# Kernel optimization log

Hardware: AMD Instinct MI355X
Metric: run time of the kernel (lower is better)

The kernel has to match this reference:

```python
import jax, jax.numpy as jnp
import numpy as np

D_LOB = 128
D_HAWKES = 32
N_HEADS = 4
HEAD_DIM = D_LOB // N_HEADS
LN_EPS = 1e-5


def setup_inputs() -> dict:
    key = jax.random.key(0)
    ks = jax.random.split(key, 10)
    B, T = 8, 2048
    s = lambda fan_in: 1.0 / np.sqrt(fan_in)
    return {
        "lob": jax.random.normal(ks[0], (B, T, D_LOB), dtype=jnp.float32),
        "hawkes": jax.random.normal(ks[1], (B, T, D_HAWKES), dtype=jnp.float32),
        # hawkes_proj: Linear(d_hawkes, d_lob)
        "Wp": jax.random.uniform(ks[2], (D_LOB, D_HAWKES), jnp.float32, -s(D_HAWKES), s(D_HAWKES)),
        "bp": jnp.zeros((D_LOB,), jnp.float32),
        # MultiheadAttention packed in-projection (3*d_lob, d_lob) and out-projection
        "Win": jax.random.uniform(ks[3], (3 * D_LOB, D_LOB), jnp.float32, -s(D_LOB), s(D_LOB)),
        "bin_": jnp.zeros((3 * D_LOB,), jnp.float32),
        "Wo": jax.random.uniform(ks[4], (D_LOB, D_LOB), jnp.float32, -s(D_LOB), s(D_LOB)),
        "bo": jnp.zeros((D_LOB,), jnp.float32),
        # LayerNorm affine params
        "gamma": jnp.ones((D_LOB,), jnp.float32),
        "beta": jnp.zeros((D_LOB,), jnp.float32),
    }


def reference(lob, hawkes, Wp, bp, Win, bin_, Wo, bo, gamma, beta):
    B, T, _ = lob.shape
    # hawkes_proj
    h = hawkes @ Wp.T + bp  # (B, T, d_lob)
    # packed QKV projection (query=lob, key=value=h)
    q = lob @ Win[:D_LOB].T + bin_[:D_LOB]
    k = h @ Win[D_LOB:2 * D_LOB].T + bin_[D_LOB:2 * D_LOB]
    v = h @ Win[2 * D_LOB:].T + bin_[2 * D_LOB:]
    # split heads -> (B, H, T, hd)
    split = lambda x: x.reshape(B, T, N_HEADS, HEAD_DIM).transpose(0, 2, 1, 3)
    q, k, v = split(q), split(k), split(v)
    scale = 1.0 / np.sqrt(HEAD_DIM).astype(np.float32)
    scores = jnp.einsum("bhqd,bhkd->bhqk", q * scale, k)  # (B, H, T, T)
    attn = jax.nn.softmax(scores, axis=-1)
    # dropout(p=0.1) omitted: reference is eval/inference mode
    ctx = jnp.einsum("bhqk,bhkd->bhqd", attn, v)  # (B, H, T, hd)
    ctx = ctx.transpose(0, 2, 1, 3).reshape(B, T, D_LOB)
    fused = ctx @ Wo.T + bo
    # residual + LayerNorm
    x = lob + fused
    mu = jnp.mean(x, axis=-1, keepdims=True)
    var = jnp.mean(jnp.square(x - mu), axis=-1, keepdims=True)
    out = (x - mu) * jax.lax.rsqrt(var + LN_EPS) * gamma + beta
    attn_w = jnp.mean(attn, axis=1)  # average over heads (B, T, T)
    return out, attn_w
```

## Files before the change

kernel.cpp:

```cpp
#include <hip/hip_runtime.h>
#include <hip/hip_bf16.h>
#include <math.h>

#define TT 2048
#define BB 8
#define DD 128
#define HH 4
#define BT (BB*TT)
#define BH (BB*HH)
#define SCALE 0.1767766952966369f
#define S2LOG (SCALE * 1.4426950408889634f)

typedef __attribute__((ext_vector_type(8))) short short8;
typedef __attribute__((ext_vector_type(4))) short short4v;
typedef __attribute__((ext_vector_type(4))) float f32x4;
typedef __attribute__((ext_vector_type(4))) unsigned u32x4;
typedef __hip_bfloat16 bf16;

#define MFMA16(a,b,c) __builtin_amdgcn_mfma_f32_16x16x32_bf16(a,b,c,0,0,0)

static __device__ inline short8 ldg8(const bf16* p) {
  return *reinterpret_cast<const short8*>(p);
}
static __device__ inline short4v ldg4(const bf16* p) {
  return *reinterpret_cast<const short4v*>(p);
}
static __device__ inline short f2bs(float x) {
  bf16 h = __float2bfloat16(x);
  return *reinterpret_cast<short*>(&h);
}
static __device__ inline unsigned cvtpk(float lo, float hi) {
  unsigned r;
  asm("v_cvt_pk_bf16_f32 %0, %1, %2" : "=v"(r) : "v"(lo), "v"(hi));
  return r;
}
static __device__ inline short8 ldcvt8(const float* p) {
  f32x4 f0 = *reinterpret_cast<const f32x4*>(p);
  f32x4 f1 = *reinterpret_cast<const f32x4*>(p + 4);
  short8 r;
  #pragma unroll
  for (int i = 0; i < 4; ++i) { r[i] = f2bs(f0[i]); r[4+i] = f2bs(f1[i]); }
  return r;
}

__global__ __launch_bounds__(256) void proj_kernel(
    const float* __restrict__ lob, const float* __restrict__ hawkes,
    const float* __restrict__ Wp, const float* __restrict__ bp,
    const float* __restrict__ Win, const float* __restrict__ binp,
    bf16* __restrict__ qg, bf16* __restrict__ kg, bf16* __restrict__ vtg) {
  __shared__ bf16 hT[32*136];
  __shared__ bf16 sK[32*136];
  __shared__ bf16 vT[128*40];
  int tid = threadIdx.x;
  int wave = tid >> 6, lane = tid & 63;
  int lr = lane & 15, lq = lane >> 4;
  int r0 = blockIdx.x * 32;
  int b  = r0 >> 11, t0 = r0 & 2047;
  f32x4 z = {0.f,0.f,0.f,0.f};

  short8 alob[2][4], ahk[2];
  #pragma unroll
  for (int mt = 0; mt < 2; ++mt) {
    const float* lp = lob + (size_t)(r0 + mt*16 + lr)*128;
    #pragma unroll
    for (int kt = 0; kt < 4; ++kt) alob[mt][kt] = ldcvt8(lp + kt*32 + lq*8);
    ahk[mt] = ldcvt8(hawkes + (size_t)(r0 + mt*16 + lr)*32 + lq*8);
  }

  for (int nt = wave; nt < 8; nt += 4) {
    int cn = nt*16;
    short8 bfrag = ldcvt8(Wp + (size_t)(cn + lr)*32 + lq*8);
    float bias = bp[cn + lr];
    #pragma unroll
    for (int mt = 0; mt < 2; ++mt) {
      f32x4 c = MFMA16(ahk[mt], bfrag, z);
      #pragma unroll
      for (int r = 0; r < 4; ++r)
        hT[(mt*16 + lq*4 + r)*136 + cn + lr] = __float2bfloat16(c[r] + bias);
    }
  }
  __syncthreads();

  short8 ah[2][4];
  #pragma unroll
  for (int mt = 0; mt < 2; ++mt)
    #pragma unroll
    for (int kt = 0; kt < 4; ++kt)
      ah[mt][kt] = *reinterpret_cast<const short8*>(&hT[(mt*16 + lr)*136 + kt*32 + lq*8]);
  __syncthreads();

  for (int nt = wave; nt < 24; nt += 4) {
    int which = nt >> 3;
    int c = (nt & 7)*16 + lr;
    const float* wrow = Win + (size_t)(which*128 + c)*128;
    float bias = binp[which*128 + c];
    f32x4 acc0 = z, acc1 = z;
    #pragma unroll
    for (int kt = 0; kt < 4; ++kt) {
      short8 bfrag = ldcvt8(wrow + kt*32 + lq*8);
      if (which == 0) {
        acc0 = MFMA16(alob[0][kt], bfrag, acc0);
        acc1 = MFMA16(alob[1][kt], bfrag, acc1);
      } else {
        acc0 = MFMA16(ah[0][kt], bfrag, acc0);
        acc1 = MFMA16(ah[1][kt], bfrag, acc1);
      }
    }
    #pragma unroll
    for (int mt = 0; mt < 2; ++mt) {
      f32x4 acc = mt ? acc1 : acc0;
      #pragma unroll
      for (int r = 0; r < 4; ++r) {
        int row = mt*16 + lq*4 + r;
        float val = acc[r] + bias;
        if (which == 0)      hT[row*136 + c] = __float2bfloat16(val);
        else if (which == 1) sK[row*136 + c] = __float2bfloat16(val);
        else                 vT[c*40 + row]  = __float2bfloat16(val);
      }
    }
  }
  __syncthreads();

  {
    int head = tid >> 6, tt = (tid >> 1) & 31, half = tid & 1;
    const bf16* sq = &hT[tt*136 + head*32 + half*16];
    const bf16* sk = &sK[tt*136 + head*32 + half*16];
    bf16* qdst = qg + ((size_t)(b*HH + head)*TT + t0 + tt)*32 + half*16;
    bf16* kdst = kg + ((size_t)(b*HH + head)*TT + t0 + tt)*32 + half*16;
    *reinterpret_cast<short8*>(qdst)     = *reinterpret_cast<const short8*>(sq);
    *reinterpret_cast<short8*>(qdst + 8) = *reinterpret_cast<const short8*>(sq + 8);
    *reinterpret_cast<short8*>(kdst)     = *reinterpret_cast<const short8*>(sk);
    *reinterpret_cast<short8*>(kdst + 8) = *reinterpret_cast<const short8*>(sk + 8);
  }
  {
    int dd = tid >> 1, half = tid & 1;
    int bh = b*HH + (dd >> 5);
    short8 s0 = *reinterpret_cast<const short8*>(&vT[dd*40 + half*16]);
    short8 s1 = *reinterpret_cast<const short8*>(&vT[dd*40 + half*16 + 8]);
    bf16* dst = vtg + ((size_t)bh*32 + (dd & 31))*TT + t0 + half*16;
    *reinterpret_cast<short8*>(dst) = s0;
    *reinterpret_cast<short8*>(dst + 8) = s1;
  }
}

__global__ __launch_bounds__(512) void attn_kernel(const bf16* __restrict__ qg,
    const bf16* __restrict__ kg, const bf16* __restrict__ vtg,
    float* __restrict__ attn_out, const float* __restrict__ lobf,
    const float* __restrict__ Wo, const float* __restrict__ bo,
    const float* __restrict__ gamma, const float* __restrict__ beta,
    float* __restrict__ outg) {
  int wgid = (blockIdx.x & 7)*64 + (blockIdx.x >> 3);
  int b = wgid >> 6, qt = wgid & 63;
  int tid = threadIdx.x;
  int wave = tid >> 6, lane = tid & 63;
  int head = wave & 3, half = wave >> 2;
  int lr = lane & 15, lq = lane >> 4;
  int bh = b*HH + head;
  __shared__ float plds[2][4][32*36];
  const bf16* qp = qg + ((size_t)bh*TT + (size_t)qt*32)*32;
  const bf16* kb = kg + (size_t)bh*TT*32;
  const bf16* vb = vtg + (size_t)bh*32*TT;
  f32x4 z = {0.f,0.f,0.f,0.f};

  short8 aq0 = ldg8(qp + lr*32 + lq*8);
  short8 aq1 = ldg8(qp + (16+lr)*32 + lq*8);

  float rs0 = 0.f, rs1 = 0.f;
  {
    short8 kA0 = ldg8(kb + (size_t)(half*32 + lr)*32 + lq*8);
    short8 kA1 = ldg8(kb + (size_t)(half*32 + 16 + lr)*32 + lq*8);
    short8 kB0, kB1;
#define P1STEP(KC0, KC1, KN0, KN1, NCC) { \
    int nc_ = (NCC); \
    KN0 = ldg8(kb + (size_t)(nc_*32 + lr)*32 + lq*8); \
    KN1 = ldg8(kb + (size_t)(nc_*32 + 16 + lr)*32 + lq*8); \
    f32x4 sa0 = MFMA16(KC0, aq0, z), sb0 = MFMA16(KC1, aq0, z); \
    f32x4 sa1 = MFMA16(KC0, aq1, z), sb1 = MFMA16(KC1, aq1, z); \
    _Pragma("unroll") for (int r = 0; r < 4; ++r) { \
      rs0 += exp2f(sa0[r]*S2LOG) + exp2f(sb0[r]*S2LOG); \
      rs1 += exp2f(sa1[r]*S2LOG) + exp2f(sb1[r]*S2LOG); } }
    #pragma unroll 1
    for (int i = 0; i < 32; i += 2) {
      P1STEP(kA0, kA1, kB0, kB1, 2*(i+1) + half);
      P1STEP(kB0, kB1, kA0, kA1, (i+2 < 32) ? 2*(i+2) + half : half);
    }
#undef P1STEP
  }
  rs0 += __shfl_xor(rs0, 16, 64); rs0 += __shfl_xor(rs0, 32, 64);
  rs1 += __shfl_xor(rs1, 16, 64); rs1 += __shfl_xor(rs1, 32, 64);
  float* sdl = &plds[0][0][0];
  if (lq == 0) { sdl[wave*32 + lr] = rs0; sdl[wave*32 + 16 + lr] = rs1; }
  __syncthreads();
  float lb0 = -log2f(sdl[head*32 + lr]      + sdl[(4+head)*32 + lr]);
  float lb1 = -log2f(sdl[head*32 + 16 + lr] + sdl[(4+head)*32 + 16 + lr]);
  __syncthreads();

  f32x4 acc00 = z, acc01 = z, acc10 = z, acc11 = z;
  float* awr = attn_out + (size_t)(b*TT + qt*32)*TT;
  int mloc = tid & 255;
  int mq = mloc >> 3, mk = (mloc & 7)*4;

  short8 kA0 = ldg8(kb + (size_t)(half*32 + lr)*32 + lq*8);
  short8 kA1 = ldg8(kb + (size_t)(half*32 + 16 + lr)*32 + lq*8);
  short4v vA00 = ldg4(vb + (size_t)lr*TT + half*32 + lq*4);
  short4v vA01 = ldg4(vb + (size_t)lr*TT + half*32 + 16 + lq*4);
  short4v vA10 = ldg4(vb + (size_t)(16+lr)*TT + half*32 + lq*4);
  short4v vA11 = ldg4(vb + (size_t)(16+lr)*TT + half*32 + 16 + lq*4);
  short8 kB0, kB1; short4v vB00, vB01, vB10, vB11;

#define P2STEP(KC, KC0, KC1, VC00, VC01, VC10, VC11, KN0, KN1, VN00, VN01, VN10, VN11, NCC) { \
    int kc_ = (KC); int nc_ = (NCC); \
    KN0 = ldg8(kb + (size_t)(nc_*32 + lr)*32 + lq*8); \
    KN1 = ldg8(kb + (size_t)(nc_*32 + 16 + lr)*32 + lq*8); \
    VN00 = ldg4(vb + (size_t)lr*TT + nc_*32 + lq*4); \
    VN01 = ldg4(vb + (size_t)lr*TT + nc_*32 + 16 + lq*4); \
    VN10 = ldg4(vb + (size_t)(16+lr)*TT + nc_*32 + lq*4); \
    VN11 = ldg4(vb + (size_t)(16+lr)*TT + nc_*32 + 16 + lq*4); \
    f32x4 s00 = MFMA16(KC0, aq0, z), s10 = MFMA16(KC1, aq0, z); \
    f32x4 s01 = MFMA16(KC0, aq1, z), s11 = MFMA16(KC1, aq1, z); \
    f32x4 p00, p10, p01, p11; \
    _Pragma("unroll") for (int r = 0; r < 4; ++r) { \
      p00[r] = exp2f(fmaf(s00[r], S2LOG, lb0)); \
      p10[r] = exp2f(fmaf(s10[r], S2LOG, lb0)); \
      p01[r] = exp2f(fmaf(s01[r], S2LOG, lb1)); \
      p11[r] = exp2f(fmaf(s11[r], S2LOG, lb1)); } \
    { float* pw = &plds[half][head][0]; \
      *reinterpret_cast<f32x4*>(pw + lr*36 + lq*4)           = p00; \
      *reinterpret_cast<f32x4*>(pw + lr*36 + 16 + lq*4)      = p10; \
      *reinterpret_cast<f32x4*>(pw + (16+lr)*36 + lq*4)      = p01; \
      *reinterpret_cast<f32x4*>(pw + (16+lr)*36 + 16 + lq*4) = p11; } \
    u32x4 ua_, ub_; \
    ua_[0] = cvtpk(p00[0], p00[1]); ua_[1] = cvtpk(p00[2], p00[3]); \
    ua_[2] = cvtpk(p10[0], p10[1]); ua_[3] = cvtpk(p10[2], p10[3]); \
    ub_[0] = cvtpk(p01[0], p01[1]); ub_[1] = cvtpk(p01[2], p01[3]); \
    ub_[2] = cvtpk(p11[0], p11[1]); ub_[3] = cvtpk(p11[2], p11[3]); \
    short8 ap0 = *reinterpret_cast<short8*>(&ua_); \
    short8 ap1 = *reinterpret_cast<short8*>(&ub_); \
    __syncthreads(); \
    { const float* pr = &plds[half][0][0]; \
      f32x4 mv = *reinterpret_cast<const f32x4*>(pr + mq*36 + mk); \
      mv = mv + *reinterpret_cast<const f32x4*>(pr + 1152 + mq*36 + mk); \
      mv = mv + *reinterpret_cast<const f32x4*>(pr + 2304 + mq*36 + mk); \
      mv = mv + *reinterpret_cast<const f32x4*>(pr + 3456 + mq*36 + mk); \
      *reinterpret_cast<f32x4*>(awr + (size_t)mq*TT + kc_*32 + mk) = mv * 0.25f; } \
    short8 vf0, vf1; \
    _Pragma("unroll") for (int j = 0; j < 4; ++j) { \
      vf0[j] = VC00[j]; vf0[4+j] = VC01[j]; \
      vf1[j] = VC10[j]; vf1[4+j] = VC11[j]; } \
    acc00 = MFMA16(ap0, vf0, acc00); acc01 = MFMA16(ap0, vf1, acc01); \
    acc10 = MFMA16(ap1, vf0, acc10); acc11 = MFMA16(ap1, vf1, acc11); \
    __syncthreads(); }

  #pragma unroll 1
  for (int i = 0; i < 32; i += 2) {
    P2STEP(2*i + half, kA0, kA1, vA00, vA01, vA10, vA11,
           kB0, kB1, vB00, vB01, vB10, vB11, 2*(i+1) + half);
    P2STEP(2*(i+1) + half, kB0, kB1, vB00, vB01, vB10, vB11,
           kA0, kA1, vA00, vA01, vA10, vA11, (i+2 < 32) ? 2*(i+2) + half : half);
  }
#undef P2STEP

  size_t rowbase = (size_t)(b*TT) + (size_t)qt*32;
  float* sRed = &plds[0][0][0];
  {
    float* myR = sRed + half*4224;
    #pragma unroll
    for (int m = 0; m < 2; ++m) {
      f32x4 a0 = m ? acc10 : acc00;
      f32x4 a1 = m ? acc11 : acc01;
      #pragma unroll
      for (int r = 0; r < 4; ++r) {
        int row = m*16 + lq*4 + r;
        myR[row*132 + head*32 + lr]      = a0[r];
        myR[row*132 + head*32 + 16 + lr] = a1[r];
      }
    }
  }
  __syncthreads();
  for (int idx = tid; idx < 4096; idx += 512) {
    int row = idx >> 7, d = idx & 127;
    sRed[row*132 + d] += sRed[4224 + row*132 + d];
  }
  __syncthreads();
  float* sX  = sRed;
  float* sX2 = sRed + 4224;
  short8 actx[2][4];
  #pragma unroll
  for (int mt = 0; mt < 2; ++mt)
    #pragma unroll
    for (int kt = 0; kt < 4; ++kt) {
      const float* cp = &sX[(mt*16 + lr)*132 + kt*32 + lq*8];
      f32x4 c0 = *reinterpret_cast<const f32x4*>(cp);
      f32x4 c1 = *reinterpret_cast<const f32x4*>(cp + 4);
      u32x4 u;
      u[0] = cvtpk(c0[0], c0[1]); u[1] = cvtpk(c0[2], c0[3]);
      u[2] = cvtpk(c1[0], c1[1]); u[3] = cvtpk(c1[2], c1[3]);
      actx[mt][kt] = *reinterpret_cast<short8*>(&u);
    }
  {
    int nt = wave;
    f32x4 acc0 = z, acc1 = z;
    #pragma unroll
    for (int kt = 0; kt < 4; ++kt) {
      short8 bfrag = ldcvt8(Wo + (size_t)(nt*16 + lr)*128 + kt*32 + lq*8);
      acc0 = MFMA16(actx[0][kt], bfrag, acc0);
      acc1 = MFMA16(actx[1][kt], bfrag, acc1);
    }
    int d = nt*16 + lr;
    float bias = bo[d];
    #pragma unroll
    for (int mt = 0; mt < 2; ++mt) {
      f32x4 acc = mt ? acc1 : acc0;
      #pragma unroll
      for (int r = 0; r < 4; ++r) {
        int row = mt*16 + lq*4 + r;
        sX2[row*132 + d] = acc[r] + bias + lobf[(rowbase + row)*128 + d];
      }
    }
  }
  __syncthreads();
  {
    int row = tid >> 4, j = tid & 15;
    const float* xp = &sX2[row*132 + j*8];
    f32x4 x0 = *reinterpret_cast<const f32x4*>(xp);
    f32x4 x1 = *reinterpret_cast<const f32x4*>(xp + 4);
    float sum = 0.f, sq = 0.f;
    #pragma unroll
    for (int e = 0; e < 4; ++e) {
      sum += x0[e] + x1[e];
      sq  += x0[e]*x0[e] + x1[e]*x1[e];
    }
    #pragma unroll
    for (int mdx = 1; mdx < 16; mdx <<= 1) {
      sum += __shfl_xor(sum, mdx, 64);
      sq  += __shfl_xor(sq,  mdx, 64);
    }
    float mu = sum * (1.0f/128.0f);
    float rstd = rsqrtf(sq*(1.0f/128.0f) - mu*mu + 1e-5f);
    float* op = outg + (rowbase + row)*128 + j*8;
    f32x4 o0, o1;
    #pragma unroll
    for (int e = 0; e < 4; ++e) {
      int d = j*8 + e;
      o0[e] = (x0[e] - mu)*rstd*gamma[d]   + beta[d];
      o1[e] = (x1[e] - mu)*rstd*gamma[d+4] + beta[d+4];
    }
    *reinterpret_cast<f32x4*>(op)     = o0;
    *reinterpret_cast<f32x4*>(op + 4) = o1;
  }
}

extern "C" void kernel_launch(void* const* d_in, const int* in_sizes, int n_in,
                              void* d_out, int out_size, void* d_ws, size_t ws_size,
                              hipStream_t stream) {
  const float* lob    = (const float*)d_in[0];
  const float* hawkes = (const float*)d_in[1];
  const float* Wp     = (const float*)d_in[2];
  const float* bp     = (const float*)d_in[3];
  const float* Win    = (const float*)d_in[4];
  const float* binp   = (const float*)d_in[5];
  const float* Wo     = (const float*)d_in[6];
  const float* bo     = (const float*)d_in[7];
  const float* gamma  = (const float*)d_in[8];
  const float* beta   = (const float*)d_in[9];
  float* outg = (float*)d_out;
  float* attn_out = outg + (size_t)BT*128;

  char* ws = (char*)d_ws;
  bf16*  qg   = (bf16*)(ws);
  bf16*  kg   = (bf16*)(ws + (size_t)4*1024*1024);
  bf16*  vtg  = (bf16*)(ws + (size_t)8*1024*1024);

  proj_kernel<<<BT/32, 256, 0, stream>>>(lob, hawkes, Wp, bp, Win, binp, qg, kg, vtg);
  attn_kernel<<<BB*(TT/32), 512, 0, stream>>>(qg, kg, vtg, attn_out,
                                              lob, Wo, bo, gamma, beta, outg);
}
```

Before: 275.6 us.

## Halve query tile to 16 rows, double-buffer bf16 probabilities in LDS, drop one barrier

Each attention workgroup now handles 16 query rows instead of 32, so the grid doubles to 1024 blocks. Per-head probabilities are stored to LDS as packed bf16 instead of fp32, and a ping-pong buffer lets each step use one barrier instead of two. The head-averaged attention weights are rebuilt from the bf16 values. This aims to improve occupancy and cut LDS traffic and sync stalls, at the cost of re-reading K and V twice as often and slightly lower precision in attn_w.

```diff
diff --git a/kernel.cpp b/kernel.cpp
--- a/kernel.cpp
+++ b/kernel.cpp
@@ -14,7 +14,9 @@
 typedef __attribute__((ext_vector_type(8))) short short8;
 typedef __attribute__((ext_vector_type(4))) short short4v;
 typedef __attribute__((ext_vector_type(4))) float f32x4;
+typedef __attribute__((ext_vector_type(2))) float f32x2;
 typedef __attribute__((ext_vector_type(4))) unsigned u32x4;
+typedef __attribute__((ext_vector_type(2))) unsigned u32x2;
 typedef __hip_bfloat16 bf16;
 
 #define MFMA16(a,b,c) __builtin_amdgcn_mfma_f32_16x16x32_bf16(a,b,c,0,0,0)
@@ -149,23 +151,22 @@
     const float* __restrict__ Wo, const float* __restrict__ bo,
     const float* __restrict__ gamma, const float* __restrict__ beta,
     float* __restrict__ outg) {
-  int wgid = (blockIdx.x & 7)*64 + (blockIdx.x >> 3);
-  int b = wgid >> 6, qt = wgid & 63;
+  int wgid = (blockIdx.x & 7)*128 + (blockIdx.x >> 3);
+  int b = wgid >> 7, qt = wgid & 127;
   int tid = threadIdx.x;
   int wave = tid >> 6, lane = tid & 63;
   int head = wave & 3, half = wave >> 2;
   int lr = lane & 15, lq = lane >> 4;
   int bh = b*HH + head;
-  __shared__ float plds[2][4][32*36];
-  const bf16* qp = qg + ((size_t)bh*TT + (size_t)qt*32)*32;
+  __shared__ unsigned plds[4608];
+  const bf16* qp = qg + ((size_t)bh*TT + (size_t)qt*16)*32;
   const bf16* kb = kg + (size_t)bh*TT*32;
   const bf16* vb = vtg + (size_t)bh*32*TT;
   f32x4 z = {0.f,0.f,0.f,0.f};
 
-  short8 aq0 = ldg8(qp + lr*32 + lq*8);
-  short8 aq1 = ldg8(qp + (16+lr)*32 + lq*8);
-
-  float rs0 = 0.f, rs1 = 0.f;
+  short8 aq = ldg8(qp + lr*32 + lq*8);
+
+  float rs = 0.f;
   {
     short8 kA0 = ldg8(kb + (size_t)(half*32 + lr)*32 + lq*8);
     short8 kA1 = ldg8(kb + (size_t)(half*32 + 16 + lr)*32 + lq*8);
@@ -174,31 +175,30 @@
     int nc_ = (NCC); \
     KN0 = ldg8(kb + (size_t)(nc_*32 + lr)*32 + lq*8); \
     KN1 = ldg8(kb + (size_t)(nc_*32 + 16 + lr)*32 + lq*8); \
-    f32x4 sa0 = MFMA16(KC0, aq0, z), sb0 = MFMA16(KC1, aq0, z); \
-    f32x4 sa1 = MFMA16(KC0, aq1, z), sb1 = MFMA16(KC1, aq1, z); \
-    _Pragma("unroll") for (int r = 0; r < 4; ++r) { \
-      rs0 += exp2f(sa0[r]*S2LOG) + exp2f(sb0[r]*S2LOG); \
-      rs1 += exp2f(sa1[r]*S2LOG) + exp2f(sb1[r]*S2LOG); } }
+    f32x4 sa = MFMA16(KC0, aq, z), sb = MFMA16(KC1, aq, z); \
+    _Pragma("unroll") for (int r = 0; r < 4; ++r) \
+      rs += exp2f(sa[r]*S2LOG) + exp2f(sb[r]*S2LOG); }
     #pragma unroll 1
-    for (int i = 0; i < 32; i += 2) {
-      P1STEP(kA0, kA1, kB0, kB1, 2*(i+1) + half);
-      P1STEP(kB0, kB1, kA0, kA1, (i+2 < 32) ? 2*(i+2) + half : half);
+    for (int s = 0; s < 32; s += 2) {
+      P1STEP(kA0, kA1, kB0, kB1, 2*(s+1) + half);
+      P1STEP(kB0, kB1, kA0, kA1, (s+2 < 32) ? 2*(s+2) + half : half);
     }
 #undef P1STEP
   }
-  rs0 += __shfl_xor(rs0, 16, 64); rs0 += __shfl_xor(rs0, 32, 64);
-  rs1 += __shfl_xor(rs1, 16, 64); rs1 += __shfl_xor(rs1, 32, 64);
-  float* sdl = &plds[0][0][0];
-  if (lq == 0) { sdl[wave*32 + lr] = rs0; sdl[wave*32 + 16 + lr] = rs1; }
-  __syncthreads();
-  float lb0 = -log2f(sdl[head*32 + lr]      + sdl[(4+head)*32 + lr]);
-  float lb1 = -log2f(sdl[head*32 + 16 + lr] + sdl[(4+head)*32 + 16 + lr]);
-  __syncthreads();
-
-  f32x4 acc00 = z, acc01 = z, acc10 = z, acc11 = z;
-  float* awr = attn_out + (size_t)(b*TT + qt*32)*TT;
-  int mloc = tid & 255;
-  int mq = mloc >> 3, mk = (mloc & 7)*4;
+  rs += __shfl_xor(rs, 16, 64);
+  rs += __shfl_xor(rs, 32, 64);
+  float* sdl = reinterpret_cast<float*>(plds);
+  if (lq == 0) sdl[wave*16 + lr] = rs;
+  __syncthreads();
+  float lb = -log2f(sdl[head*16 + lr] + sdl[(4+head)*16 + lr]);
+  __syncthreads();
+
+  f32x4 acc0 = z, acc1 = z;
+  float* awr = attn_out + (size_t)(b*TT + qt*16)*TT;
+  int mrow = tid >> 5, mcp = tid & 31;
+  const unsigned* pmean = plds + (mcp >> 4)*1152 + mrow*18 + (mcp & 15);
+  float* awm = awr + (size_t)mrow*TT + mcp*2;
+  unsigned* pw = plds + half*1152 + head*288;
 
   short8 kA0 = ldg8(kb + (size_t)(half*32 + lr)*32 + lq*8);
   short8 kA1 = ldg8(kb + (size_t)(half*32 + 16 + lr)*32 + lq*8);
@@ -208,145 +208,119 @@
   short4v vA11 = ldg4(vb + (size_t)(16+lr)*TT + half*32 + 16 + lq*4);
   short8 kB0, kB1; short4v vB00, vB01, vB10, vB11;
 
-#define P2STEP(KC, KC0, KC1, VC00, VC01, VC10, VC11, KN0, KN1, VN00, VN01, VN10, VN11, NCC) { \
-    int kc_ = (KC); int nc_ = (NCC); \
+#define P2STEP(SI, KC0, KC1, VC00, VC01, VC10, VC11, KN0, KN1, VN00, VN01, VN10, VN11, NCC) { \
+    int nc_ = (NCC); \
     KN0 = ldg8(kb + (size_t)(nc_*32 + lr)*32 + lq*8); \
     KN1 = ldg8(kb + (size_t)(nc_*32 + 16 + lr)*32 + lq*8); \
     VN00 = ldg4(vb + (size_t)lr*TT + nc_*32 + lq*4); \
     VN01 = ldg4(vb + (size_t)lr*TT + nc_*32 + 16 + lq*4); \
     VN10 = ldg4(vb + (size_t)(16+lr)*TT + nc_*32 + lq*4); \
     VN11 = ldg4(vb + (size_t)(16+lr)*TT + nc_*32 + 16 + lq*4); \
-    f32x4 s00 = MFMA16(KC0, aq0, z), s10 = MFMA16(KC1, aq0, z); \
-    f32x4 s01 = MFMA16(KC0, aq1, z), s11 = MFMA16(KC1, aq1, z); \
-    f32x4 p00, p10, p01, p11; \
+    f32x4 s0 = MFMA16(KC0, aq, z), s1 = MFMA16(KC1, aq, z); \
+    f32x4 p0, p1; \
     _Pragma("unroll") for (int r = 0; r < 4; ++r) { \
-      p00[r] = exp2f(fmaf(s00[r], S2LOG, lb0)); \
-      p10[r] = exp2f(fmaf(s10[r], S2LOG, lb0)); \
-      p01[r] = exp2f(fmaf(s01[r], S2LOG, lb1)); \
-      p11[r] = exp2f(fmaf(s11[r], S2LOG, lb1)); } \
-    { float* pw = &plds[half][head][0]; \
-      *reinterpret_cast<f32x4*>(pw + lr*36 + lq*4)           = p00; \
-      *reinterpret_cast<f32x4*>(pw + lr*36 + 16 + lq*4)      = p10; \
-      *reinterpret_cast<f32x4*>(pw + (16+lr)*36 + lq*4)      = p01; \
-      *reinterpret_cast<f32x4*>(pw + (16+lr)*36 + 16 + lq*4) = p11; } \
-    u32x4 ua_, ub_; \
-    ua_[0] = cvtpk(p00[0], p00[1]); ua_[1] = cvtpk(p00[2], p00[3]); \
-    ua_[2] = cvtpk(p10[0], p10[1]); ua_[3] = cvtpk(p10[2], p10[3]); \
-    ub_[0] = cvtpk(p01[0], p01[1]); ub_[1] = cvtpk(p01[2], p01[3]); \
-    ub_[2] = cvtpk(p11[0], p11[1]); ub_[3] = cvtpk(p11[2], p11[3]); \
-    short8 ap0 = *reinterpret_cast<short8*>(&ua_); \
-    short8 ap1 = *reinterpret_cast<short8*>(&ub_); \
-    __syncthreads(); \
-    { const float* pr = &plds[half][0][0]; \
-      f32x4 mv = *reinterpret_cast<const f32x4*>(pr + mq*36 + mk); \
-      mv = mv + *reinterpret_cast<const f32x4*>(pr + 1152 + mq*36 + mk); \
-      mv = mv + *reinterpret_cast<const f32x4*>(pr + 2304 + mq*36 + mk); \
-      mv = mv + *reinterpret_cast<const f32x4*>(pr + 3456 + mq*36 + mk); \
-      *reinterpret_cast<f32x4*>(awr + (size_t)mq*TT + kc_*32 + mk) = mv * 0.25f; } \
+      p0[r] = exp2f(fmaf(s0[r], S2LOG, lb)); \
+      p1[r] = exp2f(fmaf(s1[r], S2LOG, lb)); } \
+    u32x4 ua; \
+    ua[0] = cvtpk(p0[0], p0[1]); ua[1] = cvtpk(p0[2], p0[3]); \
+    ua[2] = cvtpk(p1[0], p1[1]); ua[3] = cvtpk(p1[2], p1[3]); \
+    { unsigned* pd = pw + ((SI)&1)*2304 + lr*18 + 2*lq; \
+      *reinterpret_cast<u32x2*>(pd)     = (u32x2){ua[0], ua[1]}; \
+      *reinterpret_cast<u32x2*>(pd + 8) = (u32x2){ua[2], ua[3]}; } \
+    short8 ap = *reinterpret_cast<short8*>(&ua); \
     short8 vf0, vf1; \
     _Pragma("unroll") for (int j = 0; j < 4; ++j) { \
       vf0[j] = VC00[j]; vf0[4+j] = VC01[j]; \
       vf1[j] = VC10[j]; vf1[4+j] = VC11[j]; } \
-    acc00 = MFMA16(ap0, vf0, acc00); acc01 = MFMA16(ap0, vf1, acc01); \
-    acc10 = MFMA16(ap1, vf0, acc10); acc11 = MFMA16(ap1, vf1, acc11); \
-    __syncthreads(); }
+    acc0 = MFMA16(ap, vf0, acc0); \
+    acc1 = MFMA16(ap, vf1, acc1); \
+    __syncthreads(); \
+    { const unsigned* pr = pmean + ((SI)&1)*2304; \
+      float m0 = 0.f, m1 = 0.f; \
+      _Pragma("unroll") for (int h = 0; h < 4; ++h) { \
+        unsigned u = pr[h*288]; \
+        m0 += __uint_as_float(u << 16); \
+        m1 += __uint_as_float(u & 0xffff0000u); } \
+      *reinterpret_cast<f32x2*>(awm + (SI)*64) = (f32x2){m0*0.25f, m1*0.25f}; } }
 
   #pragma unroll 1
-  for (int i = 0; i < 32; i += 2) {
-    P2STEP(2*i + half, kA0, kA1, vA00, vA01, vA10, vA11,
-           kB0, kB1, vB00, vB01, vB10, vB11, 2*(i+1) + half);
-    P2STEP(2*(i+1) + half, kB0, kB1, vB00, vB01, vB10, vB11,
-           kA0, kA1, vA00, vA01, vA10, vA11, (i+2 < 32) ? 2*(i+2) + half : half);
+  for (int s = 0; s < 32; s += 2) {
+    P2STEP(s,   kA0, kA1, vA00, vA01, vA10, vA11,
+                kB0, kB1, vB00, vB01, vB10, vB11, 2*(s+1) + half);
+    P2STEP(s+1, kB0, kB1, vB00, vB01, vB10, vB11,
+                kA0, kA1, vA00, vA01, vA10, vA11, (s+2 < 32) ? 2*(s+2) + half : half);
   }
 #undef P2STEP
 
-  size_t rowbase = (size_t)(b*TT) + (size_t)qt*32;
-  float* sRed = &plds[0][0][0];
-  {
-    float* myR = sRed + half*4224;
-    #pragma unroll
-    for (int m = 0; m < 2; ++m) {
-      f32x4 a0 = m ? acc10 : acc00;
-      f32x4 a1 = m ? acc11 : acc01;
-      #pragma unroll
-      for (int r = 0; r < 4; ++r) {
-        int row = m*16 + lq*4 + r;
-        myR[row*132 + head*32 + lr]      = a0[r];
-        myR[row*132 + head*32 + 16 + lr] = a1[r];
-      }
-    }
-  }
-  __syncthreads();
-  for (int idx = tid; idx < 4096; idx += 512) {
+  __syncthreads();
+  size_t rowbase = (size_t)(b*TT) + (size_t)qt*16;
+  float* sRed = reinterpret_cast<float*>(plds);
+  {
+    float* myR = sRed + half*2112;
+    #pragma unroll
+    for (int r = 0; r < 4; ++r) {
+      int row = lq*4 + r;
+      myR[row*132 + head*32 + lr]      = acc0[r];
+      myR[row*132 + head*32 + 16 + lr] = acc1[r];
+    }
+  }
+  __syncthreads();
+  for (int idx = tid; idx < 2048; idx += 512) {
     int row = idx >> 7, d = idx & 127;
-    sRed[row*132 + d] += sRed[4224 + row*132 + d];
+    sRed[row*132 + d] += sRed[2112 + row*132 + d];
   }
   __syncthreads();
   float* sX  = sRed;
-  float* sX2 = sRed + 4224;
-  short8 actx[2][4];
+  float* sX2 = sRed + 2112;
+  short8 actx[4];
   #pragma unroll
-  for (int mt = 0; mt < 2; ++mt)
-    #pragma unroll
-    for (int kt = 0; kt < 4; ++kt) {
-      const float* cp = &sX[(mt*16 + lr)*132 + kt*32 + lq*8];
-      f32x4 c0 = *reinterpret_cast<const f32x4*>(cp);
-      f32x4 c1 = *reinterpret_cast<const f32x4*>(cp + 4);
-      u32x4 u;
-      u[0] = cvtpk(c0[0], c0[1]); u[1] = cvtpk(c0[2], c0[3]);
-      u[2] = cvtpk(c1[0], c1[1]); u[3] = cvtpk(c1[2], c1[3]);
-      actx[mt][kt] = *reinterpret_cast<short8*>(&u);
-    }
+  for (int kt = 0; kt < 4; ++kt) {
+    const float* cp = &sX[lr*132 + kt*32 + lq*8];
+    f32x4 c0 = *reinterpret_cast<const f32x4*>(cp);
+    f32x4 c1 = *reinterpret_cast<const f32x4*>(cp + 4);
+    u32x4 u;
+    u[0] = cvtpk(c0[0], c0[1]); u[1] = cvtpk(c0[2], c0[3]);
+    u[2] = cvtpk(c1[0], c1[1]); u[3] = cvtpk(c1[2], c1[3]);
+    actx[kt] = *reinterpret_cast<short8*>(&u);
+  }
   {
     int nt = wave;
-    f32x4 acc0 = z, acc1 = z;
+    f32x4 acc = z;
     #pragma unroll
     for (int kt = 0; kt < 4; ++kt) {
       short8 bfrag = ldcvt8(Wo + (size_t)(nt*16 + lr)*128 + kt*32 + lq*8);
-      acc0 = MFMA16(actx[0][kt], bfrag, acc0);
-      acc1 = MFMA16(actx[1][kt], bfrag, acc1);
+      acc = MFMA16(actx[kt], bfrag, acc);
     }
     int d = nt*16 + lr;
     float bias = bo[d];
     #pragma unroll
-    for (int mt = 0; mt < 2; ++mt) {
-      f32x4 acc = mt ? acc1 : acc0;
-      #pragma unroll
-      for (int r = 0; r < 4; ++r) {
-        int row = mt*16 + lq*4 + r;
-        sX2[row*132 + d] = acc[r] + bias + lobf[(rowbase + row)*128 + d];
-      }
-    }
-  }
-  __syncthreads();
-  {
-    int row = tid >> 4, j = tid & 15;
-    const float* xp = &sX2[row*132 + j*8];
-    f32x4 x0 = *reinterpret_cast<const f32x4*>(xp);
-    f32x4 x1 = *reinterpret_cast<const f32x4*>(xp + 4);
-    float sum = 0.f, sq = 0.f;
-    #pragma unroll
-    for (int e = 0; e < 4; ++e) {
-      sum += x0[e] + x1[e];
-      sq  += x0[e]*x0[e] + x1[e]*x1[e];
-    }
-    #pragma unroll
-    for (int mdx = 1; mdx < 16; mdx <<= 1) {
+    for (int r = 0; r < 4; ++r) {
+      int row = lq*4 + r;
+      sX2[row*132 + d] = acc[r] + bias + lobf[(rowbase + row)*128 + d];
+    }
+  }
+  __syncthreads();
+  {
+    int row = tid >> 5, j = tid & 31;
+    const float* xp = &sX2[row*132 + j*4];
+    f32x4 x = *reinterpret_cast<const f32x4*>(xp);
+    float sum = x[0] + x[1] + x[2] + x[3];
+    float sq  = x[0]*x[0] + x[1]*x[1] + x[2]*x[2] + x[3]*x[3];
+    #pragma unroll
+    for (int mdx = 1; mdx < 32; mdx <<= 1) {
       sum += __shfl_xor(sum, mdx, 64);
       sq  += __shfl_xor(sq,  mdx, 64);
     }
     float mu = sum * (1.0f/128.0f);
     float rstd = rsqrtf(sq*(1.0f/128.0f) - mu*mu + 1e-5f);
-    float* op = outg + (rowbase + row)*128 + j*8;
-    f32x4 o0, o1;
+    float* op = outg + (rowbase + row)*128 + j*4;
+    f32x4 o;
     #pragma unroll
     for (int e = 0; e < 4; ++e) {
-      int d = j*8 + e;
-      o0[e] = (x0[e] - mu)*rstd*gamma[d]   + beta[d];
-      o1[e] = (x1[e] - mu)*rstd*gamma[d+4] + beta[d+4];
-    }
-    *reinterpret_cast<f32x4*>(op)     = o0;
-    *reinterpret_cast<f32x4*>(op + 4) = o1;
+      int d = j*4 + e;
+      o[e] = (x[e] - mu)*rstd*gamma[d] + beta[d];
+    }
+    *reinterpret_cast<f32x4*>(op) = o;
   }
 }
 
@@ -372,6 +346,6 @@
   bf16*  vtg  = (bf16*)(ws + (size_t)8*1024*1024);
 
   proj_kernel<<<BT/32, 256, 0, stream>>>(lob, hawkes, Wp, bp, Win, binp, qg, kg, vtg);
-  attn_kernel<<<BB*(TT/32), 512, 0, stream>>>(qg, kg, vtg, attn_out,
+  attn_kernel<<<BB*(TT/16), 512, 0, stream>>>(qg, kg, vtg, attn_out,
                                               lob, Wo, bo, gamma, beta, outg);
 }
```

Measured after the change: 352.3 us. 27.8% more time.
